# Kernel tuning notes

Measured on AMD Instinct MI355X. Metric: run time of the kernel, lower is better.

Reference implementation:

```python
import jax, jax.numpy as jnp
import numpy as np
import math

B, T, C = 4, 2048, 1024
NH = 16
HD = C // NH


def setup_inputs() -> dict:
    key = jax.random.key(0)
    ks = jax.random.split(key, 10)
    s = 0.02
    x = jax.random.normal(ks[0], (B, T, C), dtype=jnp.float32)
    W_qkv = jax.random.normal(ks[1], (C, 3 * C), dtype=jnp.float32) * s
    b_qkv = jnp.zeros((3 * C,), dtype=jnp.float32)
    W_proj = jax.random.normal(ks[2], (C, C), dtype=jnp.float32) * s
    b_proj = jnp.zeros((C,), dtype=jnp.float32)
    asym_mean, asym_std = 1.0, 0.7
    q_scale = jax.random.normal(ks[3], (NH, HD), dtype=jnp.float32) * asym_std + asym_mean
    q_bias = jax.random.normal(ks[4], (NH, HD), dtype=jnp.float32) * asym_std + asym_mean
    k_scale = jax.random.normal(ks[5], (NH, HD), dtype=jnp.float32) * asym_std + asym_mean
    k_bias = jax.random.normal(ks[6], (NH, HD), dtype=jnp.float32) * asym_std + asym_mean
    return {"x": x, "W_qkv": W_qkv, "b_qkv": b_qkv, "W_proj": W_proj,
            "b_proj": b_proj, "q_scale": q_scale, "q_bias": q_bias,
            "k_scale": k_scale, "k_bias": k_bias}


def reference(x, W_qkv, b_qkv, W_proj, b_proj, q_scale, q_bias, k_scale, k_bias):
    Bx, Tx, Cx = x.shape
    qkv = x @ W_qkv + b_qkv                       # [B,T,3C]
    q, k, v = jnp.split(qkv, 3, axis=-1)
    # [B,T,C] -> [B,NH,T,HD]
    reshape = lambda t: t.reshape(Bx, Tx, NH, HD).transpose(0, 2, 1, 3)
    q, k, v = reshape(q), reshape(k), reshape(v)
    # per-head affine scaling of Q/K
    q = q * q_scale[None, :, None, :] + q_bias[None, :, None, :]
    k = k * k_scale[None, :, None, :] + k_bias[None, :, None, :]
    scores = jnp.einsum('bhqd,bhkd->bhqk', q, k) / math.sqrt(HD)  # [B,NH,T,T]
    causal = jnp.tril(jnp.ones((Tx, Tx), dtype=bool))
    scores = jnp.where(causal[None, None], scores, -jnp.inf)
    att = jax.nn.softmax(scores, axis=-1)
    y = jnp.einsum('bhqk,bhkd->bhqd', att, v)     # [B,NH,T,HD]
    y = y.transpose(0, 2, 1, 3).reshape(Bx, Tx, Cx)
    return y @ W_proj + b_proj
```

## Files before the change

### kernel.cpp

```cpp
#include <hip/hip_runtime.h>
#include <hip/hip_bf16.h>

typedef unsigned short u16;
typedef __attribute__((ext_vector_type(8))) short short8;
typedef __attribute__((ext_vector_type(4))) float floatx4;

#define B_SZ 4
#define T_SZ 2048
#define C_SZ 1024
#define NH_SZ 16
#define HD_SZ 64
#define M_TOT 8192
#define K_DIM 1024

#define QSCALE 0.1803368801111204f

#define OFF_XB   ((size_t)16)
#define OFF_WQT  (OFF_XB + 8388608)
#define OFF_WPT  (OFF_WQT + 3145728)
#define OFF_PB   (OFF_WPT + 1048576)
#define OFF_Q    (OFF_PB + 8192)
#define OFF_K    (OFF_Q + 8388608)
#define OFF_V    (OFF_K + 8388608)
#define OFF_Y    (OFF_V + 8388608)
#define PB_BQKV  0
#define PB_BPROJ 3072
#define PB_QSC   4096
#define PB_QBI   5120
#define PB_KSC   6144
#define PB_KBI   7168

__device__ __forceinline__ float bf2f(u16 u) {
    return __uint_as_float(((unsigned)u) << 16);
}
__device__ __forceinline__ u16 f2bf(float f) {
    unsigned x = __float_as_uint(f);
    unsigned r = (x + 0x7fffu + ((x >> 16) & 1u)) >> 16;
    return (u16)r;
}
__device__ __forceinline__ u16 f2bf_fast(float f) {
    return (u16)((__float_as_uint(f) + 0x8000u) >> 16);
}
__device__ __forceinline__ void gl_lds16(const u16* g, u16* l) {
    __builtin_amdgcn_global_load_lds(
        (const __attribute__((address_space(1))) void*)g,
        (__attribute__((address_space(3))) void*)l, 16, 0, 0);
}
__device__ __forceinline__ int detect_isf(const u16* xx, int lane) {
    float v0 = fabsf(bf2f(xx[lane * 2]));
    float v1 = fabsf(bf2f(xx[lane * 2 + 1]));
    int b0 = (v0 > 1024.0f) || (v0 != 0.0f && v0 < 9.5367431640625e-7f);
    int b1 = (v1 > 1024.0f) || (v1 != 0.0f && v1 < 9.5367431640625e-7f);
    unsigned long long ba = __ballot(b0), bb = __ballot(b1);
    return (__popcll(ba) + __popcll(bb)) > 8;
}

__global__ __launch_bounds__(256) void prep_k(
        const void* __restrict__ x,
        const void* __restrict__ Wqkv, const void* __restrict__ Wproj,
        const void* __restrict__ bqkv, const void* __restrict__ bproj,
        const void* __restrict__ qsc, const void* __restrict__ qbi,
        const void* __restrict__ ksc, const void* __restrict__ kbi,
        u16* __restrict__ xb, u16* __restrict__ Wt_qkv,
        u16* __restrict__ Wt_proj, u16* __restrict__ pb,
        int* __restrict__ flag) {
    __shared__ u16 t[32][33];
    const int blk = blockIdx.x;
    const int isf = detect_isf((const u16*)x, threadIdx.x & 63);
    if (blk == 0 && threadIdx.x == 0) flag[0] = isf;
    if (blk < 8192) {
        const int i = blk * 256 + threadIdx.x;
        if (isf) {
            const float4 v = ((const float4*)x)[i];
            ushort4 o;
            o.x = f2bf(v.x); o.y = f2bf(v.y); o.z = f2bf(v.z); o.w = f2bf(v.w);
            ((ushort4*)xb)[i] = o;
        } else {
            ((ushort4*)xb)[i] = ((const ushort4*)x)[i];
        }
        return;
    }
    if (blk < 8200) {
        const int i4 = (blk - 8192) * 256 + threadIdx.x;
        if (i4 >= 2048) return;
        const int e = i4 * 4;
        const void* src; int off;
        if (e < 3072)      { src = bqkv;  off = e; }
        else if (e < 4096) { src = bproj; off = e - 3072; }
        else if (e < 5120) { src = qsc;   off = e - 4096; }
        else if (e < 6144) { src = qbi;   off = e - 5120; }
        else if (e < 7168) { src = ksc;   off = e - 6144; }
        else               { src = kbi;   off = e - 7168; }
        ushort4 o;
        if (isf) {
            const float4 v = *(const float4*)((const float*)src + off);
            o.x = f2bf(v.x); o.y = f2bf(v.y); o.z = f2bf(v.z); o.w = f2bf(v.w);
        } else {
            o = *(const ushort4*)((const u16*)src + off);
        }
        *(ushort4*)&pb[e] = o;
        return;
    }
    const void* in; u16* out; int R, C, idx;
    if (blk < 11272) { idx = blk - 8200;  in = Wqkv;  out = Wt_qkv;  R = 1024; C = 3072; }
    else             { idx = blk - 11272; in = Wproj; out = Wt_proj; R = 1024; C = 1024; }
    const int nbx = C >> 5;
    const int c0 = (idx % nbx) * 32, r0 = (idx / nbx) * 32;
    const int tx = threadIdx.x & 31, ty = threadIdx.x >> 5;
    for (int i = 0; i < 4; i++) {
        int r = ty + i * 8;
        size_t gi = (size_t)(r0 + r) * C + c0 + tx;
        t[r][tx] = isf ? f2bf(((const float*)in)[gi]) : ((const u16*)in)[gi];
    }
    __syncthreads();
    for (int i = 0; i < 4; i++) {
        int cr = ty + i * 8;
        out[(size_t)(c0 + cr) * R + r0 + tx] = t[tx][cr];
    }
}

__global__ __launch_bounds__(256) void qkv_gemm(
        const u16* __restrict__ X, const u16* __restrict__ Wt,
        const u16* __restrict__ pb,
        u16* __restrict__ Qb, u16* __restrict__ Kb, u16* __restrict__ Vb) {
    __shared__ __align__(16) u16 As[128 * 64];
    __shared__ __align__(16) u16 Bs[128 * 64];
    const int bm = blockIdx.y * 128, bn = blockIdx.x * 128;
    const int tid = threadIdx.x;
    const int lane = tid & 63, wave = tid >> 6;
    const int quad = lane >> 4, l16 = lane & 15;
    const int wm = (wave & 1) * 64, wn = (wave >> 1) * 64;
    const int lrow = lane >> 3;
    const int lcol = ((lane & 7) ^ lrow) * 8;

    floatx4 acc[4][4];
    for (int mi = 0; mi < 4; mi++)
        for (int ni = 0; ni < 4; ni++) acc[mi][ni] = 0.f;

    for (int k0 = 0; k0 < K_DIM; k0 += 64) {
        __syncthreads();
        for (int j = 0; j < 4; j++) {
            const int rb = wave * 32 + j * 8;
            gl_lds16(&X[(size_t)(bm + rb + lrow) * K_DIM + k0 + lcol], &As[rb * 64]);
            gl_lds16(&Wt[(size_t)(bn + rb + lrow) * K_DIM + k0 + lcol], &Bs[rb * 64]);
        }
        __syncthreads();
        for (int kk = 0; kk < 64; kk += 32) {
            const int cb = kk >> 3;
            const int slot = ((cb + quad) ^ (l16 & 7)) * 8;
            short8 a[4], b[4];
            for (int mi = 0; mi < 4; mi++)
                a[mi] = *(const short8*)&As[(wm + mi * 16 + l16) * 64 + slot];
            for (int ni = 0; ni < 4; ni++)
                b[ni] = *(const short8*)&Bs[(wn + ni * 16 + l16) * 64 + slot];
            for (int mi = 0; mi < 4; mi++)
                for (int ni = 0; ni < 4; ni++)
                    acc[mi][ni] = __builtin_amdgcn_mfma_f32_16x16x32_bf16(
                        a[mi], b[ni], acc[mi][ni], 0, 0, 0);
        }
    }

    const int sec = bn >> 10;
    const int bb = bm >> 11;
    const int tbase = bm & 2047;
    for (int mi = 0; mi < 4; mi++) {
        for (int ni = 0; ni < 4; ni++) {
            const int col = bn + wn + ni * 16 + l16;
            const int cmod = col & 1023;
            const int h = cmod >> 6, d = cmod & 63;
            const float bv = bf2f(pb[PB_BQKV + col]);
            if (sec == 2) {
                const int t0 = tbase + wm + mi * 16 + quad * 4;
                ushort4 pk;
                pk.x = f2bf(acc[mi][ni][0] + bv);
                pk.y = f2bf(acc[mi][ni][1] + bv);
                pk.z = f2bf(acc[mi][ni][2] + bv);
                pk.w = f2bf(acc[mi][ni][3] + bv);
                *(ushort4*)&Vb[(((size_t)(bb * NH_SZ + h)) * HD_SZ + d) * T_SZ + t0] = pk;
            } else {
                float sA, sB;
                if (sec == 0) {
                    sA = bf2f(pb[PB_QSC + h * 64 + d]) * QSCALE;
                    sB = bf2f(pb[PB_QBI + h * 64 + d]) * QSCALE;
                } else {
                    sA = bf2f(pb[PB_KSC + h * 64 + d]);
                    sB = bf2f(pb[PB_KBI + h * 64 + d]);
                }
                u16* dstbuf = (sec == 0) ? Qb : Kb;
                for (int r = 0; r < 4; r++) {
                    const int t = tbase + wm + mi * 16 + quad * 4 + r;
                    float v = (acc[mi][ni][r] + bv) * sA + sB;
                    dstbuf[(((size_t)(bb * NH_SZ + h)) * T_SZ + t) * HD_SZ + d] = f2bf(v);
                }
            }
        }
    }
}

__global__ __launch_bounds__(512) void attn_k(const u16* __restrict__ Qb,
                                              const u16* __restrict__ Kb,
                                              const u16* __restrict__ Vtg,
                                              u16* __restrict__ Y) {
    __shared__ __align__(16) u16 Ks[64 * 64];
    __shared__ __align__(16) u16 Vs[64 * 64];
    __shared__ __align__(16) u16 Ps[8 * 16 * 88];
    const int blk = blockIdx.x;
    const int head = blk & 63;
    const int p = blk >> 6;
    const int b = head >> 4, h = head & 15;
    const int tid = threadIdx.x, lane = tid & 63, w = tid >> 6;
    const int quad = lane >> 4, l16 = lane & 15;
    const size_t qk_off = (size_t)head * (T_SZ * HD_SZ);
    const size_t v_off = (size_t)head * (HD_SZ * T_SZ);
    u16* psw = &Ps[w * 1408];
    const int lr = lane >> 3;
    const int lc = ((lane & 7) ^ lr) * 8;
    const int sl0 = ((quad) ^ (l16 & 7)) * 8;
    const int sl1 = ((4 + quad) ^ (l16 & 7)) * 8;

    short8 ones;
    for (int j = 0; j < 8; j++) ones[j] = (short)0x3F80;

    for (int tile = 0; tile < 2; tile++) {
        const int qt = tile ? p : (15 - p);
        const int q0 = qt * 128;
        const int rbase = q0 + w * 16;
        const int q = rbase + l16;

        const short8 aq0 = *(const short8*)&Qb[qk_off + (size_t)q * HD_SZ + quad * 8];
        const short8 aq1 = *(const short8*)&Qb[qk_off + (size_t)q * HD_SZ + 32 + quad * 8];

        floatx4 o[4];
        for (int mi = 0; mi < 4; mi++) o[mi] = 0.f;
        float m_run = -1e30f, l_run = 0.f;

        for (int k0 = 0; k0 < q0 + 128; k0 += 64) {
            __syncthreads();
            gl_lds16(&Kb[qk_off + (size_t)(k0 + w * 8 + lr) * HD_SZ + lc], &Ks[w * 512]);
            gl_lds16(&Vtg[v_off + (size_t)(w * 8 + lr) * T_SZ + k0 + lc], &Vs[w * 512]);
            __syncthreads();
            if (k0 > rbase + 15) continue;

            floatx4 s[4];
            for (int ni = 0; ni < 4; ni++) s[ni] = 0.f;
            for (int ni = 0; ni < 4; ni++)
                s[ni] = __builtin_amdgcn_mfma_f32_16x16x32_bf16(
                    *(const short8*)&Ks[(ni * 16 + l16) * 64 + sl0], aq0, s[ni], 0, 0, 0);
            for (int ni = 0; ni < 4; ni++)
                s[ni] = __builtin_amdgcn_mfma_f32_16x16x32_bf16(
                    *(const short8*)&Ks[(ni * 16 + l16) * 64 + sl1], aq1, s[ni], 0, 0, 0);

            if (k0 + 63 > rbase) {
                for (int ni = 0; ni < 4; ni++)
                    for (int r = 0; r < 4; r++) {
                        int key = k0 + ni * 16 + quad * 4 + r;
                        if (key > q) s[ni][r] = -1e30f;
                    }
            }

            float mx = fmaxf(fmaxf(s[0][0], s[0][1]), fmaxf(s[0][2], s[0][3]));
            for (int ni = 1; ni < 4; ni++)
                mx = fmaxf(mx, fmaxf(fmaxf(s[ni][0], s[ni][1]),
                                     fmaxf(s[ni][2], s[ni][3])));
            mx = fmaxf(mx, __shfl_xor(mx, 16, 64));
            mx = fmaxf(mx, __shfl_xor(mx, 32, 64));
            const float mnew = fmaxf(m_run, mx);
            const float alpha = exp2f(m_run - mnew);
            for (int ni = 0; ni < 4; ni++)
                for (int r = 0; r < 4; r++)
                    s[ni][r] = exp2f(s[ni][r] - mnew);
            m_run = mnew;
            for (int mi = 0; mi < 4; mi++) o[mi] *= alpha;

            for (int ni = 0; ni < 4; ni++) {
                ushort4 pk;
                pk.x = f2bf_fast(s[ni][0]); pk.y = f2bf_fast(s[ni][1]);
                pk.z = f2bf_fast(s[ni][2]); pk.w = f2bf_fast(s[ni][3]);
                *(ushort4*)&psw[l16 * 88 + ni * 16 + quad * 4] = pk;
            }

            floatx4 s4 = 0.f;
            for (int kk = 0; kk < 64; kk += 32) {
                short8 pfr = *(const short8*)&psw[l16 * 88 + kk + quad * 8];
                const int vsl = (kk == 0) ? sl0 : sl1;
                s4 = __builtin_amdgcn_mfma_f32_16x16x32_bf16(ones, pfr, s4, 0, 0, 0);
                for (int mi = 0; mi < 4; mi++) {
                    short8 vfr = *(const short8*)&Vs[(mi * 16 + l16) * 64 + vsl];
                    o[mi] = __builtin_amdgcn_mfma_f32_16x16x32_bf16(vfr, pfr, o[mi], 0, 0, 0);
                }
            }
            l_run = l_run * alpha + s4[0];
        }

        const float inv = 1.0f / l_run;
        u16* yrow = &Y[(((size_t)b * T_SZ + q) * NH_SZ + h) * HD_SZ];
        for (int mi = 0; mi < 4; mi++) {
            ushort4 pk;
            pk.x = f2bf_fast(o[mi][0] * inv); pk.y = f2bf_fast(o[mi][1] * inv);
            pk.z = f2bf_fast(o[mi][2] * inv); pk.w = f2bf_fast(o[mi][3] * inv);
            *(ushort4*)&yrow[mi * 16 + quad * 4] = pk;
        }
    }
}

__global__ __launch_bounds__(256) void proj_gemm(const u16* __restrict__ Yin,
                                                 const u16* __restrict__ Wt,
                                                 const u16* __restrict__ pb,
                                                 void* __restrict__ out,
                                                 const int* __restrict__ flag) {
    __shared__ __align__(16) u16 As[128 * 64];
    __shared__ __align__(16) u16 Bs[128 * 64];
    const int isf = flag[0];
    const int bm = blockIdx.y * 128, bn = blockIdx.x * 128;
    const int tid = threadIdx.x;
    const int lane = tid & 63, wave = tid >> 6;
    const int quad = lane >> 4, l16 = lane & 15;
    const int wm = (wave & 1) * 64, wn = (wave >> 1) * 64;
    const int lrow = lane >> 3;
    const int lcol = ((lane & 7) ^ lrow) * 8;

    floatx4 acc[4][4];
    for (int mi = 0; mi < 4; mi++)
        for (int ni = 0; ni < 4; ni++) acc[mi][ni] = 0.f;

    for (int k0 = 0; k0 < K_DIM; k0 += 64) {
        __syncthreads();
        for (int j = 0; j < 4; j++) {
            const int rb = wave * 32 + j * 8;
            gl_lds16(&Yin[(size_t)(bm + rb + lrow) * K_DIM + k0 + lcol], &As[rb * 64]);
            gl_lds16(&Wt[(size_t)(bn + rb + lrow) * K_DIM + k0 + lcol], &Bs[rb * 64]);
        }
        __syncthreads();
        for (int kk = 0; kk < 64; kk += 32) {
            const int cb = kk >> 3;
            const int slot = ((cb + quad) ^ (l16 & 7)) * 8;
            short8 a[4], b[4];
            for (int mi = 0; mi < 4; mi++)
                a[mi] = *(const short8*)&As[(wm + mi * 16 + l16) * 64 + slot];
            for (int ni = 0; ni < 4; ni++)
                b[ni] = *(const short8*)&Bs[(wn + ni * 16 + l16) * 64 + slot];
            for (int mi = 0; mi < 4; mi++)
                for (int ni = 0; ni < 4; ni++)
                    acc[mi][ni] = __builtin_amdgcn_mfma_f32_16x16x32_bf16(
                        a[mi], b[ni], acc[mi][ni], 0, 0, 0);
        }
    }

    for (int mi = 0; mi < 4; mi++) {
        for (int ni = 0; ni < 4; ni++) {
            const int col = bn + wn + ni * 16 + l16;
            const float bv = bf2f(pb[PB_BPROJ + col]);
            for (int r = 0; r < 4; r++) {
                const int row = bm + wm + mi * 16 + quad * 4 + r;
                const float v = acc[mi][ni][r] + bv;
                if (isf) ((float*)out)[(size_t)row * C_SZ + col] = v;
                else     ((u16*)out)[(size_t)row * C_SZ + col] = f2bf(v);
            }
        }
    }
}

extern "C" void kernel_launch(void* const* d_in, const int* in_sizes, int n_in,
                              void* d_out, int out_size, void* d_ws, size_t ws_size,
                              hipStream_t stream) {
    const void* x     = d_in[0];
    const void* Wqkv  = d_in[1];
    const void* bqkv  = d_in[2];
    const void* Wproj = d_in[3];
    const void* bproj = d_in[4];
    const void* qsc   = d_in[5];
    const void* qbi   = d_in[6];
    const void* ksc   = d_in[7];
    const void* kbi   = d_in[8];

    u16* ws = (u16*)d_ws;
    int* flag    = (int*)d_ws;
    u16* xb      = ws + OFF_XB;
    u16* Wt_qkv  = ws + OFF_WQT;
    u16* Wt_proj = ws + OFF_WPT;
    u16* pb      = ws + OFF_PB;
    u16* Qb      = ws + OFF_Q;
    u16* Kb      = ws + OFF_K;
    u16* Vb      = ws + OFF_V;
    u16* Yb      = ws + OFF_Y;

    prep_k<<<12296, 256, 0, stream>>>(x, Wqkv, Wproj, bqkv, bproj,
                                      qsc, qbi, ksc, kbi,
                                      xb, Wt_qkv, Wt_proj, pb, flag);
    qkv_gemm<<<dim3(24, 64), 256, 0, stream>>>(xb, Wt_qkv, pb, Qb, Kb, Vb);
    attn_k<<<dim3(512), 512, 0, stream>>>(Qb, Kb, Vb, Yb);
    proj_gemm<<<dim3(8, 64), 256, 0, stream>>>(Yb, Wt_proj, pb, d_out, flag);
}
```

Measured before the change: 307.5 us.

## Double-buffer QKV GEMM with larger 256x192 tiles and 512-thread blocks

Rewrites the QKV projection GEMM to use 256x192 block tiles with 8 waves, double-buffered LDS, and async global-to-LDS prefetch two k-steps ahead. Waits use explicit vmcnt/lgkmcnt counters and raw barriers, and s_setprio is raised around MFMA bursts. The goal is to overlap memory loads with matrix math and to reuse each loaded operand across more output elements. The cost is larger LDS use (about 112 KB per block) and more accumulator registers, which may lower occupancy. The hand-tuned waitcnt values also rely on a fixed count of outstanding loads.

```diff
diff --git a/kernel.cpp b/kernel.cpp
--- a/kernel.cpp
+++ b/kernel.cpp
@@ -119,57 +119,110 @@
     }
 }
 
-__global__ __launch_bounds__(256) void qkv_gemm(
+#define QG_BM 256
+#define QG_BN 192
+#define QG_NT 16
+
+__global__ __launch_bounds__(512, 2) void qkv_gemm(
         const u16* __restrict__ X, const u16* __restrict__ Wt,
         const u16* __restrict__ pb,
         u16* __restrict__ Qb, u16* __restrict__ Kb, u16* __restrict__ Vb) {
-    __shared__ __align__(16) u16 As[128 * 64];
-    __shared__ __align__(16) u16 Bs[128 * 64];
-    const int bm = blockIdx.y * 128, bn = blockIdx.x * 128;
+    __shared__ __align__(16) u16 As[2][QG_BM * 64];
+    __shared__ __align__(16) u16 Bs[2][QG_BN * 64];
+    const int bm = blockIdx.y * QG_BM, bn = blockIdx.x * QG_BN;
     const int tid = threadIdx.x;
-    const int lane = tid & 63, wave = tid >> 6;
+    const int lane = tid & 63, w = tid >> 6;
     const int quad = lane >> 4, l16 = lane & 15;
-    const int wm = (wave & 1) * 64, wn = (wave >> 1) * 64;
+    const int wm = (w >> 2) * 128;
+    const int wn = (w & 3) * 48;
     const int lrow = lane >> 3;
     const int lcol = ((lane & 7) ^ lrow) * 8;
-
-    floatx4 acc[4][4];
-    for (int mi = 0; mi < 4; mi++)
-        for (int ni = 0; ni < 4; ni++) acc[mi][ni] = 0.f;
-
-    for (int k0 = 0; k0 < K_DIM; k0 += 64) {
-        __syncthreads();
-        for (int j = 0; j < 4; j++) {
-            const int rb = wave * 32 + j * 8;
-            gl_lds16(&X[(size_t)(bm + rb + lrow) * K_DIM + k0 + lcol], &As[rb * 64]);
-            gl_lds16(&Wt[(size_t)(bn + rb + lrow) * K_DIM + k0 + lcol], &Bs[rb * 64]);
-        }
-        __syncthreads();
-        for (int kk = 0; kk < 64; kk += 32) {
-            const int cb = kk >> 3;
-            const int slot = ((cb + quad) ^ (l16 & 7)) * 8;
-            short8 a[4], b[4];
-            for (int mi = 0; mi < 4; mi++)
-                a[mi] = *(const short8*)&As[(wm + mi * 16 + l16) * 64 + slot];
-            for (int ni = 0; ni < 4; ni++)
-                b[ni] = *(const short8*)&Bs[(wn + ni * 16 + l16) * 64 + slot];
-            for (int mi = 0; mi < 4; mi++)
-                for (int ni = 0; ni < 4; ni++)
-                    acc[mi][ni] = __builtin_amdgcn_mfma_f32_16x16x32_bf16(
-                        a[mi], b[ni], acc[mi][ni], 0, 0, 0);
-        }
-    }
-
-    const int sec = bn >> 10;
+    const int sl0 = ((0 + quad) ^ (l16 & 7)) * 8;
+    const int sl1 = ((4 + quad) ^ (l16 & 7)) * 8;
+
+#define QG_STAGE(slot, kt) do {                                                  \
+        const int k0_ = (kt) * 64;                                               \
+        _Pragma("unroll")                                                        \
+        for (int j = 0; j < 4; j++) {                                            \
+            const int rb = w * 32 + j * 8;                                       \
+            gl_lds16(&X[(size_t)(bm + rb + lrow) * K_DIM + k0_ + lcol],          \
+                     &As[slot][rb * 64]);                                        \
+        }                                                                        \
+        _Pragma("unroll")                                                        \
+        for (int j = 0; j < 3; j++) {                                            \
+            const int rb = w * 24 + j * 8;                                       \
+            gl_lds16(&Wt[(size_t)(bn + rb + lrow) * K_DIM + k0_ + lcol],         \
+                     &Bs[slot][rb * 64]);                                        \
+        }                                                                        \
+    } while (0)
+
+    floatx4 acc[8][3];
+#pragma unroll
+    for (int mi = 0; mi < 8; mi++)
+#pragma unroll
+        for (int ni = 0; ni < 3; ni++) acc[mi][ni] = 0.f;
+
+    QG_STAGE(0, 0);
+    QG_STAGE(1, 1);
+    asm volatile("s_waitcnt vmcnt(7)" ::: "memory");
+    __builtin_amdgcn_s_barrier();
+
+    for (int t = 0; t < QG_NT; ++t) {
+        const int cur = t & 1;
+        const u16* as = As[cur];
+        const u16* bs = Bs[cur];
+        short8 a[8], b[3];
+#pragma unroll
+        for (int mi = 0; mi < 8; mi++)
+            a[mi] = *(const short8*)&as[(wm + mi * 16 + l16) * 64 + sl0];
+#pragma unroll
+        for (int ni = 0; ni < 3; ni++)
+            b[ni] = *(const short8*)&bs[(wn + ni * 16 + l16) * 64 + sl0];
+        __builtin_amdgcn_s_setprio(1);
+#pragma unroll
+        for (int mi = 0; mi < 8; mi++)
+#pragma unroll
+            for (int ni = 0; ni < 3; ni++)
+                acc[mi][ni] = __builtin_amdgcn_mfma_f32_16x16x32_bf16(
+                    a[mi], b[ni], acc[mi][ni], 0, 0, 0);
+        __builtin_amdgcn_s_setprio(0);
+#pragma unroll
+        for (int mi = 0; mi < 8; mi++)
+            a[mi] = *(const short8*)&as[(wm + mi * 16 + l16) * 64 + sl1];
+#pragma unroll
+        for (int ni = 0; ni < 3; ni++)
+            b[ni] = *(const short8*)&bs[(wn + ni * 16 + l16) * 64 + sl1];
+        asm volatile("s_waitcnt lgkmcnt(0)" ::: "memory");
+        __builtin_amdgcn_s_barrier();
+        if (t < QG_NT - 1) {
+            const int tn = (t + 2 < QG_NT) ? t + 2 : QG_NT - 1;
+            QG_STAGE(cur, tn);
+        }
+        __builtin_amdgcn_s_setprio(1);
+#pragma unroll
+        for (int mi = 0; mi < 8; mi++)
+#pragma unroll
+            for (int ni = 0; ni < 3; ni++)
+                acc[mi][ni] = __builtin_amdgcn_mfma_f32_16x16x32_bf16(
+                    a[mi], b[ni], acc[mi][ni], 0, 0, 0);
+        __builtin_amdgcn_s_setprio(0);
+        asm volatile("s_waitcnt vmcnt(7)" ::: "memory");
+        __builtin_amdgcn_s_barrier();
+    }
+#undef QG_STAGE
+
     const int bb = bm >> 11;
     const int tbase = bm & 2047;
-    for (int mi = 0; mi < 4; mi++) {
-        for (int ni = 0; ni < 4; ni++) {
-            const int col = bn + wn + ni * 16 + l16;
-            const int cmod = col & 1023;
-            const int h = cmod >> 6, d = cmod & 63;
-            const float bv = bf2f(pb[PB_BQKV + col]);
-            if (sec == 2) {
+#pragma unroll
+    for (int ni = 0; ni < 3; ni++) {
+        const int col = bn + wn + ni * 16 + l16;
+        const int sec = col >> 10;
+        const int cmod = col & 1023;
+        const int h = cmod >> 6, d = cmod & 63;
+        const float bv = bf2f(pb[PB_BQKV + col]);
+        if (sec == 2) {
+#pragma unroll
+            for (int mi = 0; mi < 8; mi++) {
                 const int t0 = tbase + wm + mi * 16 + quad * 4;
                 ushort4 pk;
                 pk.x = f2bf(acc[mi][ni][0] + bv);
@@ -177,22 +230,25 @@
                 pk.z = f2bf(acc[mi][ni][2] + bv);
                 pk.w = f2bf(acc[mi][ni][3] + bv);
                 *(ushort4*)&Vb[(((size_t)(bb * NH_SZ + h)) * HD_SZ + d) * T_SZ + t0] = pk;
+            }
+        } else {
+            float sA, sB;
+            if (sec == 0) {
+                sA = bf2f(pb[PB_QSC + h * 64 + d]) * QSCALE;
+                sB = bf2f(pb[PB_QBI + h * 64 + d]) * QSCALE;
             } else {
-                float sA, sB;
-                if (sec == 0) {
-                    sA = bf2f(pb[PB_QSC + h * 64 + d]) * QSCALE;
-                    sB = bf2f(pb[PB_QBI + h * 64 + d]) * QSCALE;
-                } else {
-                    sA = bf2f(pb[PB_KSC + h * 64 + d]);
-                    sB = bf2f(pb[PB_KBI + h * 64 + d]);
+                sA = bf2f(pb[PB_KSC + h * 64 + d]);
+                sB = bf2f(pb[PB_KBI + h * 64 + d]);
+            }
+            u16* dstbuf = (sec == 0) ? Qb : Kb;
+#pragma unroll
+            for (int mi = 0; mi < 8; mi++)
+#pragma unroll
+                for (int r = 0; r < 4; r++) {
+                    const int tt = tbase + wm + mi * 16 + quad * 4 + r;
+                    float v = (acc[mi][ni][r] + bv) * sA + sB;
+                    dstbuf[(((size_t)(bb * NH_SZ + h)) * T_SZ + tt) * HD_SZ + d] = f2bf(v);
                 }
-                u16* dstbuf = (sec == 0) ? Qb : Kb;
-                for (int r = 0; r < 4; r++) {
-                    const int t = tbase + wm + mi * 16 + quad * 4 + r;
-                    float v = (acc[mi][ni][r] + bv) * sA + sB;
-                    dstbuf[(((size_t)(bb * NH_SZ + h)) * T_SZ + t) * HD_SZ + d] = f2bf(v);
-                }
-            }
         }
     }
 }
@@ -387,7 +443,7 @@
     prep_k<<<12296, 256, 0, stream>>>(x, Wqkv, Wproj, bqkv, bproj,
                                       qsc, qbi, ksc, kbi,
                                       xb, Wt_qkv, Wt_proj, pb, flag);
-    qkv_gemm<<<dim3(24, 64), 256, 0, stream>>>(xb, Wt_qkv, pb, Qb, Kb, Vb);
+    qkv_gemm<<<dim3(16, 32), 512, 0, stream>>>(xb, Wt_qkv, pb, Qb, Kb, Vb);
     attn_k<<<dim3(512), 512, 0, stream>>>(Qb, Kb, Vb, Yb);
     proj_gemm<<<dim3(8, 64), 256, 0, stream>>>(Yb, Wt_proj, pb, d_out, flag);
 }
```

New measurement: 297.5 us. -3.2%, faster.
